# Optimization experiments

Measured on AMD Instinct MI355X. Metric: run time of the kernel, lower is better.

Reference implementation:

```python
import jax, jax.numpy as jnp
import numpy as np

H, K, V, F = 8, 64, 192, 192  # heads, key_size, value_size, num_position_features


def central_mask_features(distances, feature_size, seq_length):
    # distances: [L] float; returns [L, feature_size]
    pow_rate = np.exp(np.log(seq_length + 1) / feature_size).astype('float32')
    center_widths = jnp.power(pow_rate, jnp.arange(1, feature_size + 1, dtype=jnp.float32)) - 1.0
    return (center_widths[None, :] > jnp.abs(distances)[:, None]).astype(jnp.float32)


def positional_features(distances, feature_size, seq_length, symmetric=False):
    num_components = 1 if symmetric else 2
    emb = central_mask_features(distances, feature_size // num_components, seq_length)
    if not symmetric:
        emb = jnp.concatenate([emb, jnp.sign(distances)[:, None] * emb], axis=-1)
    return emb  # [L, feature_size]


def relative_shift(x):
    # x: [B, H, T1, T2] with T2 = 2*T1 - 1 -> [B, H, T1, T1]
    b, h, t1, t2 = x.shape
    x = jnp.pad(x, ((0, 0), (0, 0), (0, 0), (1, 0)))  # [B,H,T1,T2+1]
    x = x.reshape(b, h, t2 + 1, t1)[:, :, 1:, :]      # drop first row
    x = x.reshape(b, h, t1, t2)
    return x[..., : (t2 + 1) // 2]


def setup_inputs() -> dict:
    key = jax.random.key(0)
    ks = jax.random.split(key, 9)
    B, T, C = 2, 1536, 1536
    s = 1.0 / np.sqrt(C).astype('float32')
    return {
        'inputs': jax.random.normal(ks[0], (B, T, C), jnp.float32),
        'Wq': jax.random.normal(ks[1], (C, H * K), jnp.float32) * s,
        'Wk': jax.random.normal(ks[2], (C, H * K), jnp.float32) * s,
        'Wv': jax.random.normal(ks[3], (C, H * V), jnp.float32) * s,
        'Wrk': jax.random.normal(ks[4], (F, H * K), jnp.float32) * (1.0 / np.sqrt(F).astype('float32')),
        'We': jax.random.normal(ks[5], (H * V, H * V), jnp.float32) * (1.0 / np.sqrt(H * V).astype('float32')),
        'be': jnp.zeros((H * V,), jnp.float32),
        'r_w_bias': jax.random.normal(ks[6], (1, H, 1, K), jnp.float32) * 0.1,
        'r_r_bias': jax.random.normal(ks[7], (1, H, 1, K), jnp.float32) * 0.1,
    }


def reference(inputs, Wq, Wk, Wv, Wrk, We, be, r_w_bias, r_r_bias):
    B, T, C = inputs.shape

    def heads(x, d):  # [B,T,H*d] -> [B,H,T,d]
        return x.reshape(B, T, H, d).transpose(0, 2, 1, 3)

    q = heads(inputs @ Wq, K) * (K ** -0.5)
    k = heads(inputs @ Wk, K)
    v = heads(inputs @ Wv, V)

    # content logits: (q + r_w_bias) k^T -> [B,H,T,T]
    content_logits = jnp.einsum('bhqk,bhmk->bhqm', q + r_w_bias, k)

    # relative position logits
    distances = jnp.arange(-T + 1, T, dtype=jnp.float32)  # [2T-1]
    pe = positional_features(distances, F, T, symmetric=False)  # [2T-1, F]
    r_k = (pe @ Wrk).reshape(2 * T - 1, H, K).transpose(1, 0, 2)  # [H, 2T-1, K]
    rel_logits = jnp.einsum('bhqk,hmk->bhqm', q + r_r_bias, r_k)  # [B,H,T,2T-1]
    rel_logits = relative_shift(rel_logits)  # [B,H,T,T]

    logits = content_logits + rel_logits
    attn = jax.nn.softmax(logits, axis=-1)
    out = jnp.einsum('bhqm,bhmv->bhqv', attn, v)  # [B,H,T,V]
    out = out.transpose(0, 2, 1, 3).reshape(B, T, H * V)
    return out @ We + be
```

## Files before the change

### kernel.cpp

```cpp
#include <hip/hip_runtime.h>
#include <math.h>

#define HB 8
#define KD 64
#define VD 192
#define BT 2
#define TT 1536
#define CC 1536
#define HK (HB*KD)
#define HV (HB*VD)
#define QKVP 2560
#define LOG2E 1.44269504088896340736f

typedef float f32x4 __attribute__((ext_vector_type(4)));
typedef __bf16 bf16x8 __attribute__((ext_vector_type(8)));

static __device__ __forceinline__ ushort f2bf(float f) {
  union { float f; uint u; } v; v.f = f;
  uint r = (v.u + 0x7FFFu + ((v.u >> 16) & 1u)) >> 16;
  return (ushort)r;
}
static __device__ __forceinline__ float bf2f(ushort u) {
  union { uint u; float f; } v; v.u = ((uint)u) << 16; return v.f;
}

static __device__ __forceinline__ f32x4 mfma_bf(bf16x8 a, bf16x8 b, f32x4 c) {
  return __builtin_amdgcn_mfma_f32_16x16x32_bf16(a, b, c, 0, 0, 0);
}

static __device__ __forceinline__ void gload_lds16(const ushort* g, ushort* l) {
  __builtin_amdgcn_global_load_lds(
      (const __attribute__((address_space(1))) unsigned int*)g,
      (__attribute__((address_space(3))) unsigned int*)l, 16, 0, 0);
}

__device__ __forceinline__ void storeC(float* p, float v) { *p = v; }
__device__ __forceinline__ void storeC(ushort* p, float v) { *p = f2bf(v); }

__global__ __launch_bounds__(256) void cast_bf16(
    const float* __restrict__ in, ushort* __restrict__ out, int n4)
{
  for (int i = blockIdx.x*blockDim.x + threadIdx.x; i < n4; i += gridDim.x*blockDim.x) {
    float4 v = ((const float4*)in)[i];
    ushort4 o; o.x = f2bf(v.x); o.y = f2bf(v.y); o.z = f2bf(v.z); o.w = f2bf(v.w);
    ((ushort4*)out)[i] = o;
  }
}

__global__ void tcast(const float* __restrict__ in, ushort* __restrict__ out, int R, int C, float scale)
{
  __shared__ float tile[32][33];
  const int bx = blockIdx.x * 32;
  const int by = blockIdx.y * 32;
  const int tx = threadIdx.x, ty = threadIdx.y;
  #pragma unroll
  for (int i = 0; i < 4; ++i)
    tile[ty + i*8][tx] = in[(size_t)(by + ty + i*8)*C + bx + tx];
  __syncthreads();
  #pragma unroll
  for (int i = 0; i < 4; ++i)
    out[(size_t)(bx + ty + i*8)*R + by + tx] = f2bf(tile[tx][ty + i*8] * scale);
}

__global__ void vtrans(const ushort* __restrict__ in, ushort* __restrict__ out)
{
  __shared__ ushort tile[32][33];
  const int bx = blockIdx.x * 32;
  const int by = blockIdx.y * 32;
  const int tx = threadIdx.x, ty = threadIdx.y;
  #pragma unroll
  for (int i = 0; i < 4; ++i)
    tile[ty + i*8][tx] = in[(size_t)(by + ty + i*8)*QKVP + 1024 + bx + tx];
  __syncthreads();
  #pragma unroll
  for (int i = 0; i < 4; ++i)
    out[(size_t)(bx + ty + i*8)*(BT*TT) + by + tx] = tile[tx][ty + i*8];
}

template<bool WITH_BIAS, typename OutT>
__global__ __launch_bounds__(256) void gemm_bf16(
    const ushort* __restrict__ A, const ushort* __restrict__ Bt,
    const float* __restrict__ bias, OutT* __restrict__ C,
    int M, int N, int Kd)
{
  __shared__ __align__(16) ushort As[128*64];
  __shared__ __align__(16) ushort Bs[128*64];
  const int t = threadIdx.x;
  const int w = t >> 6, lane = t & 63;
  const int lrow = lane & 15, lk8 = lane >> 4;
  const int row0 = blockIdx.y * 128, col0 = blockIdx.x * 128;
  const int wr = (w >> 1) * 64, wc = (w & 1) * 64;

  f32x4 acc[4][4];
  #pragma unroll
  for (int m = 0; m < 4; ++m)
    #pragma unroll
    for (int n = 0; n < 4; ++n) acc[m][n] = (f32x4){0.f,0.f,0.f,0.f};

  for (int k0 = 0; k0 < Kd; k0 += 64) {
    __syncthreads();
    #pragma unroll
    for (int j = 0; j < 4; ++j) {
      const int c = (w*4 + j)*64 + lane;
      const int r = c >> 3, cp = c & 7;
      const int sc = cp ^ (r & 7);
      gload_lds16(A  + (size_t)(row0 + r)*Kd + k0 + sc*8, As + c*8);
      gload_lds16(Bt + (size_t)(col0 + r)*Kd + k0 + sc*8, Bs + c*8);
    }
    __syncthreads();
    bf16x8 af[4][2], bfv[4][2];
    #pragma unroll
    for (int m = 0; m < 4; ++m) {
      const int r = wr + m*16 + lrow;
      #pragma unroll
      for (int kh = 0; kh < 2; ++kh) {
        const int k8 = lk8 + kh*4;
        af[m][kh] = *(const bf16x8*)&As[r*64 + ((k8 ^ (r & 7)) << 3)];
      }
    }
    #pragma unroll
    for (int n = 0; n < 4; ++n) {
      const int r = wc + n*16 + lrow;
      #pragma unroll
      for (int kh = 0; kh < 2; ++kh) {
        const int k8 = lk8 + kh*4;
        bfv[n][kh] = *(const bf16x8*)&Bs[r*64 + ((k8 ^ (r & 7)) << 3)];
      }
    }
    #pragma unroll
    for (int m = 0; m < 4; ++m)
      #pragma unroll
      for (int n = 0; n < 4; ++n) {
        acc[m][n] = mfma_bf(af[m][0], bfv[n][0], acc[m][n]);
        acc[m][n] = mfma_bf(af[m][1], bfv[n][1], acc[m][n]);
      }
  }
  #pragma unroll
  for (int m = 0; m < 4; ++m)
    #pragma unroll
    for (int n = 0; n < 4; ++n) {
      const int cg = col0 + wc + n*16 + lrow;
      const float bb = WITH_BIAS ? bias[cg] : 0.f;
      #pragma unroll
      for (int r = 0; r < 4; ++r) {
        const int rg = row0 + wr + m*16 + lk8*4 + r;
        storeC(&C[(size_t)rg*N + cg], acc[m][n][r] + bb);
      }
    }
}

__global__ __launch_bounds__(256) void wrk_suffix(
    const float* __restrict__ Wrk, float* __restrict__ S1, float* __restrict__ S2)
{
  const int c = blockIdx.x*blockDim.x + threadIdx.x;
  float a1 = 0.f, a2 = 0.f;
  S1[96*HK + c] = 0.f; S2[96*HK + c] = 0.f;
  for (int i = 95; i >= 0; --i) {
    a1 += Wrk[i*HK + c];
    a2 += Wrk[(96 + i)*HK + c];
    S1[i*HK + c] = a1; S2[i*HK + c] = a2;
  }
}

__global__ __launch_bounds__(256) void relk_fill(
    const float* __restrict__ S1, const float* __restrict__ S2,
    const float* __restrict__ rrb, ushort* __restrict__ rk, float* __restrict__ c2g)
{
  __shared__ float cw[96];
  __shared__ float red[512];
  __shared__ int i0s;
  const int t = threadIdx.x;
  const int m = blockIdx.x;
  if (t < 96) {
    double pr = exp(log((double)(TT + 1)) / 96.0);
    float prf = (float)pr;
    cw[t] = (float)pow((double)prf, (double)(t + 1)) - 1.0f;
  }
  __syncthreads();
  const int d = m - (TT - 1);
  const float ad = fabsf((float)d);
  if (t == 0) {
    int i0 = 96;
    for (int i = 0; i < 96; ++i) if (cw[i] > ad) { i0 = i; break; }
    i0s = i0;
  }
  __syncthreads();
  const float sg = (d > 0) ? 1.f : (d < 0 ? -1.f : 0.f);
  const int i0 = i0s;
  for (int c = t; c < HK; c += 256) {
    const float val = S1[i0*HK + c] + sg * S2[i0*HK + c];
    const ushort vb = f2bf(val);
    rk[(size_t)m * HK + c] = vb;
    red[c] = bf2f(vb) * rrb[c];
  }
  __syncthreads();
  if (t < 8) {
    float s = 0.f;
    #pragma unroll 16
    for (int i = 0; i < 64; ++i) s += red[t*64 + i];
    c2g[(size_t)t*(2*TT - 1) + m] = s * LOG2E;
  }
}

__global__ __launch_bounds__(256) void c1_kernel(
    const ushort* __restrict__ qkv, const float* __restrict__ rwb, float* __restrict__ c1g)
{
  const int idx = blockIdx.x*256 + threadIdx.x;
  const int h = idx & 7, row = idx >> 3;
  const ushort* kr = &qkv[(size_t)row*QKVP + 512 + h*KD];
  float s = 0.f;
  #pragma unroll 16
  for (int c = 0; c < 64; ++c) s += bf2f(kr[c]) * rwb[h*KD + c];
  c1g[h*(BT*TT) + row] = s * LOG2E;
}

__global__ __launch_bounds__(256, 2) void attn_mfma(
    const ushort* __restrict__ qkv, const ushort* __restrict__ vTg,
    const ushort* __restrict__ rk,
    const float* __restrict__ c1g, const float* __restrict__ c2g,
    ushort* __restrict__ aout)
{
  __shared__ __align__(16) ushort ktL[64*64];
  __shared__ __align__(16) ushort rkbL[96*64];
  __shared__ __align__(16) ushort vTl[192*64];
  __shared__ __align__(16) ushort Pl[32][72];
  __shared__ __align__(16) float S1[32][68];
  __shared__ __align__(16) float S2[32][98];
  __shared__ float corrl[32], linv[32];

  const int t = threadIdx.x;
  const int wv = t >> 6, lane = t & 63;
  const int lrow = lane & 15, lk8 = lane >> 4;
  const int bid = blockIdx.x;
  const int qt = bid >> 4;
  const int h  = bid & 7;
  const int b  = (bid >> 3) & 1;
  const int q0 = qt * 32;

  bf16x8 af00, af01, af10, af11;
  {
    const ushort* qbase = &qkv[((size_t)(b*TT) + q0 + lrow)*QKVP + h*KD];
    af00 = *(const bf16x8*)&qbase[lk8*8];
    af01 = *(const bf16x8*)&qbase[32 + lk8*8];
    af10 = *(const bf16x8*)&qbase[16*QKVP + lk8*8];
    af11 = *(const bf16x8*)&qbase[16*QKVP + 32 + lk8*8];
  }

  if (t < 32) ((uint*)rkbL)[95*32 + t] = 0;

  const ushort* ksrc[2]; ushort* kdst[2];
  #pragma unroll
  for (int W = 0; W < 2; ++W) {
    const int c = W*256 + t;
    const int r = c >> 3, cp = c & 7;
    ksrc[W] = qkv + (size_t)(b*TT + r)*QKVP + 512 + h*KD + (cp ^ (r & 7))*8;
    kdst[W] = ktL + c*8;
  }
  const ushort* rsrc[3]; ushort* rdst[3];
  #pragma unroll
  for (int W = 0; W < 3; ++W) {
    const int c = W*256 + t;
    const int r = c >> 3, cp = c & 7;
    rsrc[W] = rk + (size_t)(1504 - q0 + r)*HK + h*KD + (cp ^ (r & 7))*8;
    rdst[W] = rkbL + c*8;
  }
  const bool rval = t < 248;
  const ushort* vsrc[6]; ushort* vdst[6];
  #pragma unroll
  for (int W = 0; W < 6; ++W) {
    const int c = W*256 + t;
    const int vd = c >> 3, cpk = c & 7;
    vsrc[W] = vTg + (size_t)(h*VD + vd)*(BT*TT) + b*TT + (cpk ^ (vd & 7))*8;
    vdst[W] = vTl + c*8;
  }

  int jk_[2], rt1_[2], j2_[3], rt2_[3];
  #pragma unroll
  for (int s = 0; s < 2; ++s) {
    const int idx = wv*2 + s;
    rt1_[s] = idx >> 2; jk_[s] = (idx & 3)*16 + lrow;
  }
  #pragma unroll
  for (int s = 0; s < 3; ++s) {
    const int idx = wv*3 + s;
    rt2_[s] = (idx >= 6) ? 1 : 0; j2_[s] = (idx - 6*rt2_[s])*16 + lrow;
  }

  f32x4 acc[2][3];
  #pragma unroll
  for (int i = 0; i < 2; ++i)
    #pragma unroll
    for (int j = 0; j < 3; ++j) acc[i][j] = (f32x4){0.f, 0.f, 0.f, 0.f};
  float m_i = -1e30f, l_i = 0.f;
  const int r_s = t >> 3;
  const int vsl = t & 7;

  float c1p[2], c2p[3];
  {
    const int mb0 = -q0 + 1504;
    #pragma unroll
    for (int s = 0; s < 2; ++s) c1p[s] = c1g[h*(BT*TT) + b*TT + jk_[s]];
    #pragma unroll
    for (int s = 0; s < 3; ++s) {
      const float v = c2g[(size_t)h*(2*TT - 1) + mb0 + (j2_[s] < 95 ? j2_[s] : 94)];
      c2p[s] = (j2_[s] < 95) ? v : 0.f;
    }
  }
  #pragma unroll
  for (int W = 0; W < 2; ++W) { gload_lds16(ksrc[W], kdst[W]); ksrc[W] += 64*QKVP; }
  gload_lds16(rsrc[0], rdst[0]);           rsrc[0] += 64*HK;
  gload_lds16(rsrc[1], rdst[1]);           rsrc[1] += 64*HK;
  if (rval) gload_lds16(rsrc[2], rdst[2]);
  rsrc[2] += 64*HK;
  #pragma unroll
  for (int W = 0; W < 6; ++W) { gload_lds16(vsrc[W], vdst[W]); vsrc[W] += 64; }

  for (int it = 0; it < 24; ++it) {
    asm volatile("s_waitcnt vmcnt(6)" ::: "memory");
    __builtin_amdgcn_s_barrier();
    #pragma unroll
    for (int s = 0; s < 2; ++s) {
      const int rt = rt1_[s], jk = jk_[s];
      const bf16x8 a0 = rt ? af10 : af00;
      const bf16x8 a1 = rt ? af11 : af01;
      bf16x8 b0 = *(const bf16x8*)&ktL[jk*64 + ((lk8 ^ (jk & 7)) << 3)];
      bf16x8 b1 = *(const bf16x8*)&ktL[jk*64 + (((lk8 + 4) ^ (jk & 7)) << 3)];
      f32x4 c0 = (f32x4){0.f, 0.f, 0.f, 0.f};
      c0 = mfma_bf(a0, b0, c0);
      c0 = mfma_bf(a1, b1, c0);
      #pragma unroll
      for (int r = 0; r < 4; ++r) S1[rt*16 + lk8*4 + r][jk] = c0[r] + c1p[s];
    }
    #pragma unroll
    for (int s = 0; s < 3; ++s) {
      const int rt = rt2_[s], j2 = j2_[s];
      const bf16x8 a0 = rt ? af10 : af00;
      const bf16x8 a1 = rt ? af11 : af01;
      bf16x8 b0 = *(const bf16x8*)&rkbL[j2*64 + ((lk8 ^ (j2 & 7)) << 3)];
      bf16x8 b1 = *(const bf16x8*)&rkbL[j2*64 + (((lk8 + 4) ^ (j2 & 7)) << 3)];
      f32x4 c0 = (f32x4){0.f, 0.f, 0.f, 0.f};
      c0 = mfma_bf(a0, b0, c0);
      c0 = mfma_bf(a1, b1, c0);
      #pragma unroll
      for (int r = 0; r < 4; ++r) S2[rt*16 + lk8*4 + r][j2] = c0[r] + c2p[s];
    }
    asm volatile("s_waitcnt lgkmcnt(0)" ::: "memory");
    __builtin_amdgcn_s_barrier();

    if (it < 23) {
      #pragma unroll
      for (int W = 0; W < 2; ++W) { gload_lds16(ksrc[W], kdst[W]); ksrc[W] += 64*QKVP; }
      gload_lds16(rsrc[0], rdst[0]);           rsrc[0] += 64*HK;
      gload_lds16(rsrc[1], rdst[1]);           rsrc[1] += 64*HK;
      if (rval) gload_lds16(rsrc[2], rdst[2]);
      rsrc[2] += 64*HK;
      const int kt0n = (it + 1) << 6;
      const int mbn = kt0n - q0 + 1504;
      #pragma unroll
      for (int s = 0; s < 2; ++s) c1p[s] = c1g[h*(BT*TT) + b*TT + kt0n + jk_[s]];
      #pragma unroll
      for (int s = 0; s < 3; ++s) {
        const float v = c2g[(size_t)h*(2*TT - 1) + mbn + (j2_[s] < 95 ? j2_[s] : 94)];
        c2p[s] = (j2_[s] < 95) ? v : 0.f;
      }
    }
    {
      float sv[8];
      #pragma unroll
      for (int i = 0; i < 8; ++i) {
        const int j = vsl*8 + i;
        sv[i] = S1[r_s][j] + S2[r_s][j - r_s + 31];
      }
      float lmax = sv[0];
      #pragma unroll
      for (int i = 1; i < 8; ++i) lmax = fmaxf(lmax, sv[i]);
      #pragma unroll
      for (int s = 1; s < 8; s <<= 1) lmax = fmaxf(lmax, __shfl_xor(lmax, s, 64));
      const bool defer = (lmax <= m_i + 8.0f);
      const float m_new = defer ? m_i : fmaxf(m_i, lmax);
      const float corr  = defer ? 1.0f : exp2f(m_i - m_new);
      float p[8];
      float lsum = 0.f;
      #pragma unroll
      for (int i = 0; i < 8; ++i) { p[i] = exp2f(sv[i] - m_new); lsum += p[i]; }
      uint4 pw;
      pw.x = (uint)f2bf(p[0]) | ((uint)f2bf(p[1]) << 16);
      pw.y = (uint)f2bf(p[2]) | ((uint)f2bf(p[3]) << 16);
      pw.z = (uint)f2bf(p[4]) | ((uint)f2bf(p[5]) << 16);
      pw.w = (uint)f2bf(p[6]) | ((uint)f2bf(p[7]) << 16);
      *(uint4*)&Pl[r_s][vsl*8] = pw;
      #pragma unroll
      for (int s = 1; s < 8; s <<= 1) lsum += __shfl_xor(lsum, s, 64);
      l_i = l_i * corr + lsum;
      m_i = m_new;
      if (vsl == 0) corrl[r_s] = corr;
    }
    if (it < 23) { asm volatile("s_waitcnt vmcnt(10)" ::: "memory"); }
    else         { asm volatile("s_waitcnt vmcnt(0)"  ::: "memory"); }
    asm volatile("s_waitcnt lgkmcnt(0)" ::: "memory");
    __builtin_amdgcn_s_barrier();

    {
      bf16x8 pa[2][2], bv[3][2];
      #pragma unroll
      for (int rt = 0; rt < 2; ++rt) {
        pa[rt][0] = *(const bf16x8*)&Pl[rt*16 + lrow][lk8*8];
        pa[rt][1] = *(const bf16x8*)&Pl[rt*16 + lrow][32 + lk8*8];
      }
      #pragma unroll
      for (int cc = 0; cc < 3; ++cc) {
        const int rv = (3*wv + cc)*16 + lrow;
        bv[cc][0] = *(const bf16x8*)&vTl[rv*64 + ((lk8 ^ (rv & 7)) << 3)];
        bv[cc][1] = *(const bf16x8*)&vTl[rv*64 + (((lk8 + 4) ^ (rv & 7)) << 3)];
      }
      float cr[2][4];
      #pragma unroll
      for (int rt = 0; rt < 2; ++rt)
        #pragma unroll
        for (int r = 0; r < 4; ++r) cr[rt][r] = corrl[rt*16 + lk8*4 + r];
      asm volatile("s_waitcnt lgkmcnt(0)" ::: "memory");
      __builtin_amdgcn_s_barrier();
      if (it < 23) {
        #pragma unroll
        for (int W = 0; W < 6; ++W) { gload_lds16(vsrc[W], vdst[W]); vsrc[W] += 64; }
      }
      bool need = false;
      #pragma unroll
      for (int rt = 0; rt < 2; ++rt)
        #pragma unroll
        for (int r = 0; r < 4; ++r) need |= (cr[rt][r] != 1.0f);
      if (__any(need ? 1 : 0)) {
        #pragma unroll
        for (int rt = 0; rt < 2; ++rt)
          #pragma unroll
          for (int cc = 0; cc < 3; ++cc)
            #pragma unroll
            for (int r = 0; r < 4; ++r) acc[rt][cc][r] *= cr[rt][r];
      }
      #pragma unroll
      for (int rt = 0; rt < 2; ++rt)
        #pragma unroll
        for (int cc = 0; cc < 3; ++cc) {
          acc[rt][cc] = mfma_bf(pa[rt][0], bv[cc][0], acc[rt][cc]);
          acc[rt][cc] = mfma_bf(pa[rt][1], bv[cc][1], acc[rt][cc]);
        }
    }
  }
  if (vsl == 0) linv[r_s] = 1.0f / l_i;
  __syncthreads();
  #pragma unroll
  for (int rt = 0; rt < 2; ++rt) {
    #pragma unroll
    for (int cc = 0; cc < 3; ++cc) {
      const int colg = (3*wv + cc)*16 + lrow;
      #pragma unroll
      for (int r = 0; r < 4; ++r) {
        const int rowg = rt*16 + lk8*4 + r;
        aout[((size_t)(b*TT) + q0 + rowg) * HV + h*VD + colg] = f2bf(acc[rt][cc][r] * linv[rowg]);
      }
    }
  }
}

extern "C" void kernel_launch(void* const* d_in, const int* in_sizes, int n_in,
                              void* d_out, int out_size, void* d_ws, size_t ws_size,
                              hipStream_t stream)
{
  const float* X   = (const float*)d_in[0];
  const float* Wq  = (const float*)d_in[1];
  const float* Wk  = (const float*)d_in[2];
  const float* Wv  = (const float*)d_in[3];
  const float* Wrk = (const float*)d_in[4];
  const float* We  = (const float*)d_in[5];
  const float* be  = (const float*)d_in[6];
  const float* rwb = (const float*)d_in[7];
  const float* rrb = (const float*)d_in[8];
  float* out = (float*)d_out;

  char* ws = (char*)d_ws;
  ushort* Xb    = (ushort*)ws;                       ws += (size_t)3072*1536*2;
  ushort* Wqkvt = (ushort*)ws;                       ws += (size_t)2560*1536*2;
  ushort* Wet   = (ushort*)ws;                       ws += (size_t)1536*1536*2;
  float*  S1b   = (float*)ws;                        ws += (size_t)97*512*4;
  float*  S2b   = (float*)ws;                        ws += (size_t)97*512*4;
  ushort* qkvb  = (ushort*)ws;                       ws += (size_t)3072*2560*2;
  ushort* vTgb  = (ushort*)ws;                       ws += (size_t)1536*3072*2;
  ushort* rkb   = (ushort*)ws;                       ws += (size_t)3071*512*2;
  float*  c1g   = (float*)ws;                        ws += (size_t)8*3072*4;
  float*  c2g   = (float*)ws;                        ws += (size_t)8*3071*4;
  ushort* ao    = (ushort*)ws;

  dim3 blk(256);
  cast_bf16<<<2048, blk, 0, stream>>>(X, Xb, (3072*1536)/4);
  tcast<<<dim3(512/32, 1536/32),  dim3(32,8), 0, stream>>>(Wq, Wqkvt,                      1536, 512,  0.125f*LOG2E);
  tcast<<<dim3(512/32, 1536/32),  dim3(32,8), 0, stream>>>(Wk, Wqkvt + (size_t)512*1536,   1536, 512,  1.0f);
  tcast<<<dim3(1536/32, 1536/32), dim3(32,8), 0, stream>>>(Wv, Wqkvt + (size_t)1024*1536,  1536, 1536, 1.0f);
  tcast<<<dim3(1536/32, 1536/32), dim3(32,8), 0, stream>>>(We, Wet, 1536, 1536, 1.0f);
  wrk_suffix<<<2, blk, 0, stream>>>(Wrk, S1b, S2b);
  relk_fill<<<dim3(2*TT - 1), blk, 0, stream>>>(S1b, S2b, rrb, rkb, c2g);
  gemm_bf16<false, ushort><<<dim3(20, 24), blk, 0, stream>>>(Xb, Wqkvt, nullptr, qkvb, 3072, QKVP, 1536);
  vtrans<<<dim3(1536/32, 3072/32), dim3(32,8), 0, stream>>>(qkvb, vTgb);
  c1_kernel<<<96, blk, 0, stream>>>(qkvb, rwb, c1g);
  attn_mfma<<<dim3(BT*HB*(TT/32)), blk, 0, stream>>>(qkvb, vTgb, rkb, c1g, c2g, ao);
  gemm_bf16<true, float><<<dim3(12, 24), blk, 0, stream>>>(ao, Wet, be, out, 3072, 1536, 1536);
}
```

Measured before the change: 216.2 us.

## Run attention with 512-thread blocks, split load and MFMA roles across eight waves

Doubles the attention block to eight waves. Each wave now owns one 16-row P·V output slice, and the QK/rel-K MFMA tiles are spread over the waves. Global-to-LDS loads are split by thread half: the first half loads rel-K and the second half loads K. The relative-logit tile is written directly into a shifted 64-column layout, so the softmax pass reads aligned float4 values with 16 lanes per row. This aims to raise latency hiding and parallelism per block, at the cost of higher per-CU LDS and register pressure under the new launch bounds, plus extra divergence from the validity guards.

```diff
diff --git a/kernel.cpp b/kernel.cpp
--- a/kernel.cpp
+++ b/kernel.cpp
@@ -214,7 +214,7 @@
   c1g[h*(BT*TT) + row] = s * LOG2E;
 }
 
-__global__ __launch_bounds__(256, 2) void attn_mfma(
+__global__ __launch_bounds__(512, 4) void attn_mfma(
     const ushort* __restrict__ qkv, const ushort* __restrict__ vTg,
     const ushort* __restrict__ rk,
     const float* __restrict__ c1g, const float* __restrict__ c2g,
@@ -225,7 +225,7 @@
   __shared__ __align__(16) ushort vTl[192*64];
   __shared__ __align__(16) ushort Pl[32][72];
   __shared__ __align__(16) float S1[32][68];
-  __shared__ __align__(16) float S2[32][98];
+  __shared__ __align__(16) float S2s[32][68];
   __shared__ float corrl[32], linv[32];
 
   const int t = threadIdx.x;
@@ -239,224 +239,188 @@
 
   bf16x8 af00, af01, af10, af11;
   {
-    const ushort* qbase = &qkv[((size_t)(b*TT) + q0 + lrow)*QKVP + h*KD];
-    af00 = *(const bf16x8*)&qbase[lk8*8];
-    af01 = *(const bf16x8*)&qbase[32 + lk8*8];
-    af10 = *(const bf16x8*)&qbase[16*QKVP + lk8*8];
-    af11 = *(const bf16x8*)&qbase[16*QKVP + 32 + lk8*8];
-  }
-
-  if (t < 32) ((uint*)rkbL)[95*32 + t] = 0;
-
-  const ushort* ksrc[2]; ushort* kdst[2];
-  #pragma unroll
-  for (int W = 0; W < 2; ++W) {
-    const int c = W*256 + t;
-    const int r = c >> 3, cp = c & 7;
-    ksrc[W] = qkv + (size_t)(b*TT + r)*QKVP + 512 + h*KD + (cp ^ (r & 7))*8;
-    kdst[W] = ktL + c*8;
-  }
-  const ushort* rsrc[3]; ushort* rdst[3];
+    const ushort* qb0 = &qkv[((size_t)(b*TT) + q0 + lrow)*QKVP + h*KD];
+    af00 = *(const bf16x8*)&qb0[lk8*8];
+    af01 = *(const bf16x8*)&qb0[32 + lk8*8];
+    af10 = *(const bf16x8*)&qb0[16*QKVP + lk8*8];
+    af11 = *(const bf16x8*)&qb0[16*QKVP + 32 + lk8*8];
+  }
+
+  int rtT[3], colT[3]; bool isS1T[3], validT[3];
+  #pragma unroll
+  for (int s = 0; s < 3; ++s) {
+    int idx = wv + 8*s;
+    validT[s] = (idx < 20);
+    if (idx > 19) idx = 19;
+    if (idx < 8) { isS1T[s] = true;  rtT[s] = idx >> 2; colT[s] = (idx & 3)*16 + lrow; }
+    else { const int k = idx - 8; isS1T[s] = false; rtT[s] = k/6; colT[s] = (k%6)*16 + lrow; }
+  }
+
+  const ushort* sp[3]; ushort* sd[3]; size_t sstep;
+  if (t < 256) {
+    sstep = (size_t)64*HK;
+    #pragma unroll
+    for (int W = 0; W < 3; ++W) {
+      const int c = W*256 + t, r = c >> 3, cp = c & 7;
+      sp[W] = rk + (size_t)(1504 - q0 + r)*HK + h*KD + (cp ^ (r & 7))*8;
+      sd[W] = rkbL + c*8;
+    }
+  } else {
+    sstep = (size_t)64*QKVP;
+    #pragma unroll
+    for (int W = 0; W < 2; ++W) {
+      const int c = W*256 + (t - 256), r = c >> 3, cp = c & 7;
+      sp[W] = qkv + (size_t)(b*TT + r)*QKVP + 512 + h*KD + (cp ^ (r & 7))*8;
+      sd[W] = ktL + c*8;
+    }
+    sp[2] = sp[0]; sd[2] = sd[0];
+  }
+  const ushort* vsrc[3]; ushort* vdst[3];
   #pragma unroll
   for (int W = 0; W < 3; ++W) {
-    const int c = W*256 + t;
-    const int r = c >> 3, cp = c & 7;
-    rsrc[W] = rk + (size_t)(1504 - q0 + r)*HK + h*KD + (cp ^ (r & 7))*8;
-    rdst[W] = rkbL + c*8;
-  }
-  const bool rval = t < 248;
-  const ushort* vsrc[6]; ushort* vdst[6];
-  #pragma unroll
-  for (int W = 0; W < 6; ++W) {
-    const int c = W*256 + t;
-    const int vd = c >> 3, cpk = c & 7;
+    const int c = W*512 + t, vd = c >> 3, cpk = c & 7;
     vsrc[W] = vTg + (size_t)(h*VD + vd)*(BT*TT) + b*TT + (cpk ^ (vd & 7))*8;
     vdst[W] = vTl + c*8;
   }
 
-  int jk_[2], rt1_[2], j2_[3], rt2_[3];
-  #pragma unroll
-  for (int s = 0; s < 2; ++s) {
-    const int idx = wv*2 + s;
-    rt1_[s] = idx >> 2; jk_[s] = (idx & 3)*16 + lrow;
-  }
+  f32x4 acc[3];
+  #pragma unroll
+  for (int j = 0; j < 3; ++j) acc[j] = (f32x4){0.f, 0.f, 0.f, 0.f};
+  float m_i = -1e30f, l_i = 0.f;
+  const int r_s = t >> 4;
+  const int c4  = (t & 15) * 4;
+
+  float cP[3];
   #pragma unroll
   for (int s = 0; s < 3; ++s) {
-    const int idx = wv*3 + s;
-    rt2_[s] = (idx >= 6) ? 1 : 0; j2_[s] = (idx - 6*rt2_[s])*16 + lrow;
-  }
-
-  f32x4 acc[2][3];
-  #pragma unroll
-  for (int i = 0; i < 2; ++i)
-    #pragma unroll
-    for (int j = 0; j < 3; ++j) acc[i][j] = (f32x4){0.f, 0.f, 0.f, 0.f};
-  float m_i = -1e30f, l_i = 0.f;
-  const int r_s = t >> 3;
-  const int vsl = t & 7;
-
-  float c1p[2], c2p[3];
-  {
-    const int mb0 = -q0 + 1504;
-    #pragma unroll
-    for (int s = 0; s < 2; ++s) c1p[s] = c1g[h*(BT*TT) + b*TT + jk_[s]];
+    if (isS1T[s]) cP[s] = c1g[h*(BT*TT) + b*TT + 0 + colT[s]];
+    else {
+      const int mb = 0 - q0 + 1504;
+      cP[s] = c2g[(size_t)h*(2*TT - 1) + mb + (colT[s] < 95 ? colT[s] : 94)];
+    }
+  }
+  #pragma unroll
+  for (int W = 0; W < 3; ++W) { gload_lds16(sp[W], sd[W]); sp[W] += sstep; }
+  #pragma unroll
+  for (int W = 0; W < 3; ++W) { gload_lds16(vsrc[W], vdst[W]); vsrc[W] += 64; }
+
+  for (int it = 0; it < 24; ++it) {
+    asm volatile("s_waitcnt vmcnt(3)" ::: "memory");
+    __builtin_amdgcn_s_barrier();
     #pragma unroll
     for (int s = 0; s < 3; ++s) {
-      const float v = c2g[(size_t)h*(2*TT - 1) + mb0 + (j2_[s] < 95 ? j2_[s] : 94)];
-      c2p[s] = (j2_[s] < 95) ? v : 0.f;
-    }
-  }
-  #pragma unroll
-  for (int W = 0; W < 2; ++W) { gload_lds16(ksrc[W], kdst[W]); ksrc[W] += 64*QKVP; }
-  gload_lds16(rsrc[0], rdst[0]);           rsrc[0] += 64*HK;
-  gload_lds16(rsrc[1], rdst[1]);           rsrc[1] += 64*HK;
-  if (rval) gload_lds16(rsrc[2], rdst[2]);
-  rsrc[2] += 64*HK;
-  #pragma unroll
-  for (int W = 0; W < 6; ++W) { gload_lds16(vsrc[W], vdst[W]); vsrc[W] += 64; }
-
-  for (int it = 0; it < 24; ++it) {
-    asm volatile("s_waitcnt vmcnt(6)" ::: "memory");
-    __builtin_amdgcn_s_barrier();
-    #pragma unroll
-    for (int s = 0; s < 2; ++s) {
-      const int rt = rt1_[s], jk = jk_[s];
-      const bf16x8 a0 = rt ? af10 : af00;
-      const bf16x8 a1 = rt ? af11 : af01;
-      bf16x8 b0 = *(const bf16x8*)&ktL[jk*64 + ((lk8 ^ (jk & 7)) << 3)];
-      bf16x8 b1 = *(const bf16x8*)&ktL[jk*64 + (((lk8 + 4) ^ (jk & 7)) << 3)];
-      f32x4 c0 = (f32x4){0.f, 0.f, 0.f, 0.f};
-      c0 = mfma_bf(a0, b0, c0);
-      c0 = mfma_bf(a1, b1, c0);
-      #pragma unroll
-      for (int r = 0; r < 4; ++r) S1[rt*16 + lk8*4 + r][jk] = c0[r] + c1p[s];
-    }
-    #pragma unroll
-    for (int s = 0; s < 3; ++s) {
-      const int rt = rt2_[s], j2 = j2_[s];
-      const bf16x8 a0 = rt ? af10 : af00;
-      const bf16x8 a1 = rt ? af11 : af01;
-      bf16x8 b0 = *(const bf16x8*)&rkbL[j2*64 + ((lk8 ^ (j2 & 7)) << 3)];
-      bf16x8 b1 = *(const bf16x8*)&rkbL[j2*64 + (((lk8 + 4) ^ (j2 & 7)) << 3)];
-      f32x4 c0 = (f32x4){0.f, 0.f, 0.f, 0.f};
-      c0 = mfma_bf(a0, b0, c0);
-      c0 = mfma_bf(a1, b1, c0);
-      #pragma unroll
-      for (int r = 0; r < 4; ++r) S2[rt*16 + lk8*4 + r][j2] = c0[r] + c2p[s];
+      if (validT[s]) {
+        const int rt = rtT[s], col = colT[s];
+        const bf16x8 a0 = rt ? af10 : af00;
+        const bf16x8 a1 = rt ? af11 : af01;
+        const ushort* base = isS1T[s] ? ktL : rkbL;
+        bf16x8 b0 = *(const bf16x8*)&base[col*64 + ((lk8 ^ (col & 7)) << 3)];
+        bf16x8 b1 = *(const bf16x8*)&base[col*64 + (((lk8 + 4) ^ (col & 7)) << 3)];
+        f32x4 c0 = (f32x4){0.f, 0.f, 0.f, 0.f};
+        c0 = mfma_bf(a0, b0, c0);
+        c0 = mfma_bf(a1, b1, c0);
+        if (isS1T[s]) {
+          #pragma unroll
+          for (int r = 0; r < 4; ++r) S1[rt*16 + lk8*4 + r][col] = c0[r] + cP[s];
+        } else {
+          #pragma unroll
+          for (int r = 0; r < 4; ++r) {
+            const int row = rt*16 + lk8*4 + r;
+            const int j = col + row - 31;
+            if (j >= 0 && j < 64) S2s[row][j] = c0[r] + cP[s];
+          }
+        }
+      }
     }
     asm volatile("s_waitcnt lgkmcnt(0)" ::: "memory");
     __builtin_amdgcn_s_barrier();
 
     if (it < 23) {
-      #pragma unroll
-      for (int W = 0; W < 2; ++W) { gload_lds16(ksrc[W], kdst[W]); ksrc[W] += 64*QKVP; }
-      gload_lds16(rsrc[0], rdst[0]);           rsrc[0] += 64*HK;
-      gload_lds16(rsrc[1], rdst[1]);           rsrc[1] += 64*HK;
-      if (rval) gload_lds16(rsrc[2], rdst[2]);
-      rsrc[2] += 64*HK;
       const int kt0n = (it + 1) << 6;
-      const int mbn = kt0n - q0 + 1504;
-      #pragma unroll
-      for (int s = 0; s < 2; ++s) c1p[s] = c1g[h*(BT*TT) + b*TT + kt0n + jk_[s]];
       #pragma unroll
       for (int s = 0; s < 3; ++s) {
-        const float v = c2g[(size_t)h*(2*TT - 1) + mbn + (j2_[s] < 95 ? j2_[s] : 94)];
-        c2p[s] = (j2_[s] < 95) ? v : 0.f;
-      }
+        if (isS1T[s]) cP[s] = c1g[h*(BT*TT) + b*TT + kt0n + colT[s]];
+        else {
+          const int mbn = kt0n - q0 + 1504;
+          cP[s] = c2g[(size_t)h*(2*TT - 1) + mbn + (colT[s] < 95 ? colT[s] : 94)];
+        }
+      }
+      #pragma unroll
+      for (int W = 0; W < 3; ++W) { gload_lds16(sp[W], sd[W]); sp[W] += sstep; }
     }
     {
-      float sv[8];
-      #pragma unroll
-      for (int i = 0; i < 8; ++i) {
-        const int j = vsl*8 + i;
-        sv[i] = S1[r_s][j] + S2[r_s][j - r_s + 31];
-      }
-      float lmax = sv[0];
-      #pragma unroll
-      for (int i = 1; i < 8; ++i) lmax = fmaxf(lmax, sv[i]);
-      #pragma unroll
-      for (int s = 1; s < 8; s <<= 1) lmax = fmaxf(lmax, __shfl_xor(lmax, s, 64));
-      const bool defer = (lmax <= m_i + 8.0f);
-      const float m_new = defer ? m_i : fmaxf(m_i, lmax);
+      const float4 s1v = *(const float4*)&S1[r_s][c4];
+      const float4 s2v = *(const float4*)&S2s[r_s][c4];
+      float sv[4] = {s1v.x + s2v.x, s1v.y + s2v.y, s1v.z + s2v.z, s1v.w + s2v.w};
+      float lm = fmaxf(fmaxf(sv[0], sv[1]), fmaxf(sv[2], sv[3]));
+      #pragma unroll
+      for (int sft = 1; sft < 16; sft <<= 1) lm = fmaxf(lm, __shfl_xor(lm, sft, 64));
+      const bool defer = (lm <= m_i + 8.0f);
+      const float m_new = defer ? m_i : fmaxf(m_i, lm);
       const float corr  = defer ? 1.0f : exp2f(m_i - m_new);
-      float p[8];
-      float lsum = 0.f;
-      #pragma unroll
-      for (int i = 0; i < 8; ++i) { p[i] = exp2f(sv[i] - m_new); lsum += p[i]; }
-      uint4 pw;
-      pw.x = (uint)f2bf(p[0]) | ((uint)f2bf(p[1]) << 16);
-      pw.y = (uint)f2bf(p[2]) | ((uint)f2bf(p[3]) << 16);
-      pw.z = (uint)f2bf(p[4]) | ((uint)f2bf(p[5]) << 16);
-      pw.w = (uint)f2bf(p[6]) | ((uint)f2bf(p[7]) << 16);
-      *(uint4*)&Pl[r_s][vsl*8] = pw;
-      #pragma unroll
-      for (int s = 1; s < 8; s <<= 1) lsum += __shfl_xor(lsum, s, 64);
-      l_i = l_i * corr + lsum;
+      const float p0 = exp2f(sv[0] - m_new), p1 = exp2f(sv[1] - m_new);
+      const float p2 = exp2f(sv[2] - m_new), p3 = exp2f(sv[3] - m_new);
+      uint2 pw;
+      pw.x = (uint)f2bf(p0) | ((uint)f2bf(p1) << 16);
+      pw.y = (uint)f2bf(p2) | ((uint)f2bf(p3) << 16);
+      *(uint2*)&Pl[r_s][c4] = pw;
+      float ls = (p0 + p1) + (p2 + p3);
+      #pragma unroll
+      for (int sft = 1; sft < 16; sft <<= 1) ls += __shfl_xor(ls, sft, 64);
+      l_i = l_i * corr + ls;
       m_i = m_new;
-      if (vsl == 0) corrl[r_s] = corr;
-    }
-    if (it < 23) { asm volatile("s_waitcnt vmcnt(10)" ::: "memory"); }
-    else         { asm volatile("s_waitcnt vmcnt(0)"  ::: "memory"); }
+      if ((t & 15) == 0) corrl[r_s] = corr;
+    }
+    if (it < 23) { asm volatile("s_waitcnt vmcnt(6)" ::: "memory"); }
+    else         { asm volatile("s_waitcnt vmcnt(0)" ::: "memory"); }
     asm volatile("s_waitcnt lgkmcnt(0)" ::: "memory");
     __builtin_amdgcn_s_barrier();
 
     {
-      bf16x8 pa[2][2], bv[3][2];
-      #pragma unroll
-      for (int rt = 0; rt < 2; ++rt) {
-        pa[rt][0] = *(const bf16x8*)&Pl[rt*16 + lrow][lk8*8];
-        pa[rt][1] = *(const bf16x8*)&Pl[rt*16 + lrow][32 + lk8*8];
-      }
+      const int rtO = wv >> 2, vb0 = (wv & 3) * 3;
+      bf16x8 pa0 = *(const bf16x8*)&Pl[rtO*16 + lrow][lk8*8];
+      bf16x8 pa1 = *(const bf16x8*)&Pl[rtO*16 + lrow][32 + lk8*8];
+      bf16x8 bv[3][2];
       #pragma unroll
       for (int cc = 0; cc < 3; ++cc) {
-        const int rv = (3*wv + cc)*16 + lrow;
+        const int rv = (vb0 + cc)*16 + lrow;
         bv[cc][0] = *(const bf16x8*)&vTl[rv*64 + ((lk8 ^ (rv & 7)) << 3)];
         bv[cc][1] = *(const bf16x8*)&vTl[rv*64 + (((lk8 + 4) ^ (rv & 7)) << 3)];
       }
-      float cr[2][4];
-      #pragma unroll
-      for (int rt = 0; rt < 2; ++rt)
-        #pragma unroll
-        for (int r = 0; r < 4; ++r) cr[rt][r] = corrl[rt*16 + lk8*4 + r];
+      float cr[4];
+      #pragma unroll
+      for (int r = 0; r < 4; ++r) cr[r] = corrl[rtO*16 + lk8*4 + r];
       asm volatile("s_waitcnt lgkmcnt(0)" ::: "memory");
       __builtin_amdgcn_s_barrier();
       if (it < 23) {
         #pragma unroll
-        for (int W = 0; W < 6; ++W) { gload_lds16(vsrc[W], vdst[W]); vsrc[W] += 64; }
-      }
-      bool need = false;
-      #pragma unroll
-      for (int rt = 0; rt < 2; ++rt)
-        #pragma unroll
-        for (int r = 0; r < 4; ++r) need |= (cr[rt][r] != 1.0f);
+        for (int W = 0; W < 3; ++W) { gload_lds16(vsrc[W], vdst[W]); vsrc[W] += 64; }
+      }
+      bool need = (cr[0] != 1.f) | (cr[1] != 1.f) | (cr[2] != 1.f) | (cr[3] != 1.f);
       if (__any(need ? 1 : 0)) {
         #pragma unroll
-        for (int rt = 0; rt < 2; ++rt)
+        for (int cc = 0; cc < 3; ++cc)
           #pragma unroll
-          for (int cc = 0; cc < 3; ++cc)
-            #pragma unroll
-            for (int r = 0; r < 4; ++r) acc[rt][cc][r] *= cr[rt][r];
-      }
-      #pragma unroll
-      for (int rt = 0; rt < 2; ++rt)
-        #pragma unroll
-        for (int cc = 0; cc < 3; ++cc) {
-          acc[rt][cc] = mfma_bf(pa[rt][0], bv[cc][0], acc[rt][cc]);
-          acc[rt][cc] = mfma_bf(pa[rt][1], bv[cc][1], acc[rt][cc]);
-        }
-    }
-  }
-  if (vsl == 0) linv[r_s] = 1.0f / l_i;
-  __syncthreads();
-  #pragma unroll
-  for (int rt = 0; rt < 2; ++rt) {
+          for (int r = 0; r < 4; ++r) acc[cc][r] *= cr[r];
+      }
+      #pragma unroll
+      for (int cc = 0; cc < 3; ++cc) {
+        acc[cc] = mfma_bf(pa0, bv[cc][0], acc[cc]);
+        acc[cc] = mfma_bf(pa1, bv[cc][1], acc[cc]);
+      }
+    }
+  }
+  if ((t & 15) == 0) linv[r_s] = 1.0f / l_i;
+  __syncthreads();
+  {
+    const int rtO = wv >> 2, vb0 = (wv & 3) * 3;
     #pragma unroll
     for (int cc = 0; cc < 3; ++cc) {
-      const int colg = (3*wv + cc)*16 + lrow;
+      const int colg = (vb0 + cc)*16 + lrow;
       #pragma unroll
       for (int r = 0; r < 4; ++r) {
-        const int rowg = rt*16 + lk8*4 + r;
-        aout[((size_t)(b*TT) + q0 + rowg) * HV + h*VD + colg] = f2bf(acc[rt][cc][r] * linv[rowg]);
+        const int rowg = rtO*16 + lk8*4 + r;
+        aout[((size_t)(b*TT) + q0 + rowg) * HV + h*VD + colg] = f2bf(acc[cc][r] * linv[rowg]);
       }
     }
   }
@@ -501,6 +465,6 @@
   gemm_bf16<false, ushort><<<dim3(20, 24), blk, 0, stream>>>(Xb, Wqkvt, nullptr, qkvb, 3072, QKVP, 1536);
   vtrans<<<dim3(1536/32, 3072/32), dim3(32,8), 0, stream>>>(qkvb, vTgb);
   c1_kernel<<<96, blk, 0, stream>>>(qkvb, rwb, c1g);
-  attn_mfma<<<dim3(BT*HB*(TT/32)), blk, 0, stream>>>(qkvb, vTgb, rkb, c1g, c2g, ao);
+  attn_mfma<<<dim3(BT*HB*(TT/32)), dim3(512), 0, stream>>>(qkvb, vTgb, rkb, c1g, c2g, ao);
   gemm_bf16<true, float><<<dim3(12, 24), blk, 0, stream>>>(ao, Wet, be, out, 3072, 1536, 1536);
 }
```

After: 265.5 us. +22.8%, slower.
